# Optimization experiments

Hardware: AMD Instinct MI355X
Metric: run time of the kernel (lower is better)

Reference implementation:

```python
import jax, jax.numpy as jnp
import numpy as np
import math

B, C, H, W = 4, 256, 64, 64
E = 96  # embed_dim
SOFTMAX_SCALE = 10.0
RESIDUAL_SCALE_INIT = 0.1


def conv1x1(w, x):
    # w: [out_c, in_c], x: [b, in_c, h, w] -> [b, out_c, h, w]
    return jnp.einsum('oc,bchw->bohw', w, x)


def setup_inputs() -> dict:
    key = jax.random.key(0)
    ks = jax.random.split(key, 12)
    s = 0.02
    return {
        'x': jax.random.normal(ks[0], (B, C, H, W), jnp.float32),
        'mask': jax.random.uniform(ks[1], (B, 1, H, W), jnp.float32),
        'ln_gamma': jnp.ones((C,), jnp.float32),
        'ln_beta': jnp.zeros((C,), jnp.float32),
        'wq': jax.random.normal(ks[2], (E, C), jnp.float32) * s,
        'wk': jax.random.normal(ks[3], (E, C), jnp.float32) * s,
        'wv': jax.random.normal(ks[4], (C, C), jnp.float32) * s,
        'w_out': jax.random.normal(ks[5], (C, C), jnp.float32) * s,
        'w_qm': jax.random.normal(ks[6], (E, 1), jnp.float32) * s,
        'wd1': jax.random.normal(ks[7], (C, 2 * C), jnp.float32) * s,
        'wd2': jax.random.normal(ks[8], (C, C), jnp.float32) * s,
        'wg': jax.random.normal(ks[9], (C, C + 1), jnp.float32) * s,
        'residual_scale': jnp.asarray(RESIDUAL_SCALE_INIT, jnp.float32),
    }


def reference(x, mask, ln_gamma, ln_beta, wq, wk, wv, w_out, w_qm, wd1, wd2, wg,
              residual_scale):
    b, c, h, w = x.shape
    n = h * w

    # ChannelLayerNorm: LayerNorm over channel dim
    mu = jnp.mean(x, axis=1, keepdims=True)
    var = jnp.mean((x - mu) ** 2, axis=1, keepdims=True)
    x_norm = (x - mu) / jnp.sqrt(var + 1e-5)
    x_norm = x_norm * ln_gamma[None, :, None, None] + ln_beta[None, :, None, None]

    # Q/K/V projections (1x1 convs), flatten to [b, n, d]
    q = conv1x1(wq, x_norm) + conv1x1(w_qm, mask)
    q = q.reshape(b, E, n).transpose(0, 2, 1)        # [b, n, E]
    k = conv1x1(wk, x_norm).reshape(b, E, n).transpose(0, 2, 1)  # [b, n, E]
    v = conv1x1(wv, x).reshape(b, c, n).transpose(0, 2, 1)       # [b, n, C]

    # cosine normalization (F.normalize with eps=1e-12)
    q = q / jnp.clip(jnp.linalg.norm(q, axis=-1, keepdims=True), 1e-12)
    k = k / jnp.clip(jnp.linalg.norm(k, axis=-1, keepdims=True), 1e-12)

    scale = SOFTMAX_SCALE / math.sqrt(E)
    attn = jnp.einsum('bqe,bke->bqk', q, k) * scale  # [b, n, n]

    # keys with mask >= 0.5 are invalid -> bias -10000
    invalid_keys = (mask.reshape(b, 1, n) >= 0.5)    # [b, 1, n]
    attn = jnp.where(invalid_keys, jnp.float32(-10000.0), attn)
    attn = jax.nn.softmax(attn, axis=-1)

    attended = jnp.einsum('bqk,bkc->bqc', attn, v)   # [b, n, C]
    attended = attended.transpose(0, 2, 1).reshape(b, c, h, w)
    attended = conv1x1(w_out, attended)

    # delta correction branch
    corr_in = jnp.concatenate([attended - x, x_norm * mask], axis=1)  # [b, 2C, h, w]
    hidden = jax.nn.gelu(conv1x1(wd1, corr_in), approximate=False)
    corrective = conv1x1(wd2, hidden)

    # MaskConditionedGate (assumed): sigmoid(1x1 conv over [corrective, mask])
    gate_in = jnp.concatenate([corrective, mask], axis=1)  # [b, C+1, h, w]
    gate = jax.nn.sigmoid(conv1x1(wg, gate_in)) * mask

    delta = jnp.tanh(residual_scale) * gate * corrective
    return x + delta
```

## Files before the change

### kernel.cpp

```cpp
#include <hip/hip_runtime.h>
#include <hip/hip_bf16.h>
#include <math.h>

#define BB 4
#define CC 256
#define NN 4096
#define EE 96
#define NTOT (BB*NN)

typedef __attribute__((ext_vector_type(8))) short bf16x8;
typedef __attribute__((ext_vector_type(4))) float f32x4;

__device__ __forceinline__ short f2bf(float x) {
    __hip_bfloat16 h = __float2bfloat16(x);
    return *reinterpret_cast<short*>(&h);
}
__device__ __forceinline__ float bf2f(short s) {
    unsigned int u = ((unsigned int)(unsigned short)s) << 16;
    float f;
    __builtin_memcpy(&f, &u, 4);
    return f;
}
__device__ __forceinline__ float gelu_exact(float v) {
    return 0.5f * v * (1.0f + erff(v * 0.70710678118654752f));
}
__device__ __forceinline__ void gld16(void* lds, const void* g) {
    __builtin_amdgcn_global_load_lds(
        (const __attribute__((address_space(1))) unsigned int*)g,
        (__attribute__((address_space(3))) unsigned int*)lds, 16, 0, 0);
}

#define OFF_WQ  0
#define OFF_WK  24576
#define OFF_WV  49152
#define OFF_WO  114688
#define OFF_WD1 180224
#define OFF_WD2 311296
#define OFF_WG  376832
#define OFF_WGL 442368
#define W16_TOTAL 442624

__global__ void wconv_kernel(const float* __restrict__ wq, const float* __restrict__ wk,
                             const float* __restrict__ wv, const float* __restrict__ wo,
                             const float* __restrict__ wd1, const float* __restrict__ wd2,
                             const float* __restrict__ wg, short* __restrict__ W16) {
    int i = blockIdx.x * 256 + threadIdx.x;
    if (i >= W16_TOTAL) return;
    float v;
    if      (i < OFF_WK)  v = wq[i];
    else if (i < OFF_WV)  v = wk[i - OFF_WK];
    else if (i < OFF_WO)  v = wv[i - OFF_WV];
    else if (i < OFF_WD1) v = wo[i - OFF_WO];
    else if (i < OFF_WD2) v = wd1[i - OFF_WD1];
    else if (i < OFF_WG)  v = wd2[i - OFF_WD2];
    else if (i < OFF_WGL) { int l = i - OFF_WG; v = wg[(l >> 8) * 257 + (l & 255)]; }
    else                  v = wg[(i - OFF_WGL) * 257 + 256];
    W16[i] = f2bf(v);
}

__global__ __launch_bounds__(256) void ln_kernel(
    const float* __restrict__ x, const float* __restrict__ gamma,
    const float* __restrict__ beta,
    short* __restrict__ Xt16, short* __restrict__ Xn16) {
    __shared__ float tile[256 * 33];
    __shared__ float psum[8][32], psq[8][32];
    __shared__ float mu_s[32], rs_s[32];
    __shared__ float gs[256], bs[256];
    const int b  = blockIdx.x >> 7;
    const int p0 = (blockIdx.x & 127) * 32;
    const int tid = threadIdx.x;
    const float* xb = x + (size_t)b * CC * NN;

    gs[tid] = gamma[tid];
    bs[tid] = beta[tid];
    #pragma unroll
    for (int i = 0; i < 8; ++i) {
        int idx = tid + i * 256;
        int c = idx >> 3, p4 = (idx & 7) * 4;
        float4 v = *(const float4*)&xb[(size_t)c * NN + p0 + p4];
        tile[c * 33 + p4]     = v.x;
        tile[c * 33 + p4 + 1] = v.y;
        tile[c * 33 + p4 + 2] = v.z;
        tile[c * 33 + p4 + 3] = v.w;
    }
    __syncthreads();
    {
        int col = tid & 31, part = tid >> 5;
        float s = 0.f, sq = 0.f;
        for (int r = part * 32; r < part * 32 + 32; ++r) {
            float v = tile[r * 33 + col];
            s += v; sq += v * v;
        }
        psum[part][col] = s; psq[part][col] = sq;
    }
    __syncthreads();
    if (tid < 32) {
        float S = 0.f, SQ = 0.f;
        #pragma unroll
        for (int j = 0; j < 8; ++j) { S += psum[j][tid]; SQ += psq[j][tid]; }
        float mu = S / 256.0f;
        float var = SQ / 256.0f - mu * mu;
        mu_s[tid] = mu;
        rs_s[tid] = rsqrtf(var + 1e-5f);
    }
    __syncthreads();
    size_t rowbase = ((size_t)b * NN + p0) * CC;
    #pragma unroll
    for (int i = 0; i < 4; ++i) {
        int idx = tid + i * 256;
        int p = idx >> 5, c8 = (idx & 31) * 8;
        float mu = mu_s[p], rcp = rs_s[p];
        bf16x8 xt, xn;
        #pragma unroll
        for (int j = 0; j < 8; ++j) {
            float v = tile[(c8 + j) * 33 + p];
            float n = (v - mu) * rcp * gs[c8 + j] + bs[c8 + j];
            xt[j] = f2bf(v); xn[j] = f2bf(n);
        }
        size_t o = rowbase + (size_t)p * CC + c8;
        *(bf16x8*)&Xt16[o] = xt;
        *(bf16x8*)&Xn16[o] = xn;
    }
}

__global__ __launch_bounds__(256) void qkproj_kernel(
    const short* __restrict__ Xn16, const short* __restrict__ W16,
    const float* __restrict__ mask, const float* __restrict__ w_qm,
    short* __restrict__ Q16, short* __restrict__ K16)
{
    const int tid = threadIdx.x;
    const int w = tid >> 6, lane = tid & 63, ln = lane & 15, quad = lane >> 4;
    const int m0 = blockIdx.x * 32 + (w & 1) * 16;
    const bool isQ = (w < 2);
    const int woff = isQ ? OFF_WQ : OFF_WK;

    f32x4 acc[6];
    #pragma unroll
    for (int i = 0; i < 6; ++i) acc[i] = (f32x4){0.f, 0.f, 0.f, 0.f};

    #pragma unroll
    for (int kt = 0; kt < 8; ++kt) {
        bf16x8 af = *(const bf16x8*)&Xn16[(size_t)(m0 + ln) * 256 + kt * 32 + quad * 8];
        #pragma unroll
        for (int nt = 0; nt < 6; ++nt) {
            bf16x8 bf = *(const bf16x8*)&W16[woff + (size_t)(nt * 16 + ln) * 256 + kt * 32 + quad * 8];
            acc[nt] = __builtin_amdgcn_mfma_f32_16x16x32_bf16(af, bf, acc[nt], 0, 0, 0);
        }
    }

    short* outp = isQ ? Q16 : K16;
    #pragma unroll
    for (int r = 0; r < 4; ++r) {
        int row = m0 + quad * 4 + r;
        float mrow = isQ ? mask[row] : 0.f;
        float vals[6];
        float ss = 0.f;
        #pragma unroll
        for (int nt = 0; nt < 6; ++nt) {
            float v = acc[nt][r];
            if (isQ) v += mrow * w_qm[nt * 16 + ln];
            vals[nt] = v;
            ss += v * v;
        }
        ss += __shfl_xor(ss, 1, 64); ss += __shfl_xor(ss, 2, 64);
        ss += __shfl_xor(ss, 4, 64); ss += __shfl_xor(ss, 8, 64);
        float sc = 1.0f / fmaxf(sqrtf(ss), 1e-12f);
        #pragma unroll
        for (int nt = 0; nt < 6; ++nt)
            outp[(size_t)row * EE + nt * 16 + ln] = f2bf(vals[nt] * sc);
    }
}

__global__ __launch_bounds__(256) void vproj_kernel(
    const short* __restrict__ Xt16, const short* __restrict__ W16,
    short* __restrict__ V16t)
{
    __shared__ short Vt[256 * 40];
    const int tid = threadIdx.x;
    const int w = tid >> 6, lane = tid & 63, ln = lane & 15, quad = lane >> 4;
    const int m0 = blockIdx.x * 32;
    const int wm = w >> 1, wn = w & 1;
    const int mrow = m0 + wm * 16;

    f32x4 acc[8];
    #pragma unroll
    for (int i = 0; i < 8; ++i) acc[i] = (f32x4){0.f, 0.f, 0.f, 0.f};

    #pragma unroll
    for (int kt = 0; kt < 8; ++kt) {
        bf16x8 af = *(const bf16x8*)&Xt16[(size_t)(mrow + ln) * 256 + kt * 32 + quad * 8];
        #pragma unroll
        for (int nt = 0; nt < 8; ++nt) {
            int col = wn * 128 + nt * 16 + ln;
            bf16x8 bf = *(const bf16x8*)&W16[OFF_WV + (size_t)col * 256 + kt * 32 + quad * 8];
            acc[nt] = __builtin_amdgcn_mfma_f32_16x16x32_bf16(af, bf, acc[nt], 0, 0, 0);
        }
    }
    #pragma unroll
    for (int nt = 0; nt < 8; ++nt) {
        int ch = wn * 128 + nt * 16 + ln;
        #pragma unroll
        for (int r = 0; r < 4; ++r)
            Vt[ch * 40 + wm * 16 + quad * 4 + r] = f2bf(acc[nt][r]);
    }
    __syncthreads();
    const int b = m0 >> 12, p0l = m0 & 4095;
    #pragma unroll
    for (int i = 0; i < 4; ++i) {
        int idx = tid + i * 256;
        int ch = idx >> 2, p8 = (idx & 3) * 8;
        *(bf16x8*)&V16t[((size_t)b * CC + ch) * NN + p0l + p8] =
            *(const bf16x8*)&Vt[ch * 40 + p8];
    }
}

__global__ __launch_bounds__(256, 4) void attn_kernel(
    const short* __restrict__ Q16, const short* __restrict__ K16,
    const short* __restrict__ V16t, const float* __restrict__ mask,
    short* __restrict__ Opart, float* __restrict__ Lpart)
{
    __shared__ short Vs[8192];
    __shared__ short Ks[3072];
    __shared__ short Ps[64 * 40];
    __shared__ float flg[32];

    const int tid = threadIdx.x;
    const int w = tid >> 6, lane = tid & 63, ln = lane & 15, quad = lane >> 4;
    const int bidx = blockIdx.x;
    const int kg = bidx >> 8;
    const int qg = bidx & 255;
    const int b  = (qg & 7) >> 1;
    const int qt = ((qg >> 3) << 1) | (qg & 1);
    const int q0 = qt * 64;
    const size_t bN = (size_t)b * NN;
    const size_t bCC = (size_t)b * CC;
    const int kbase = kg * 1024;
    const float C1 = 1.02062072615966f;
    const int wbase = w * 64;

    bf16x8 qf[3];
    #pragma unroll
    for (int e = 0; e < 3; ++e)
        qf[e] = *(const bf16x8*)&Q16[(bN + q0 + w * 16 + ln) * EE + e * 32 + quad * 8];

    f32x4 acc[4][4];
    #pragma unroll
    for (int mt = 0; mt < 4; ++mt)
        #pragma unroll
        for (int nt = 0; nt < 4; ++nt) acc[mt][nt] = (f32x4){0.f, 0.f, 0.f, 0.f};
    float lsum[4] = {0.f, 0.f, 0.f, 0.f};

    gld16(&Ks[wbase * 8], &K16[(bN + kbase + (tid & 31)) * EE + (tid >> 5) * 8]);
    if (w < 2)
        gld16(&Ks[(256 + wbase) * 8],
              &K16[(bN + kbase + (tid & 31)) * EE + (8 + (tid >> 5)) * 8]);
    if (w == 3 && lane < 8)
        gld16(&flg[0], &mask[bN + kbase + lane * 4]);
    __syncthreads();

    for (int it = 0; it < 32; ++it) {
        const int k0 = kbase + it * 32;
        #pragma unroll
        for (int i = 0; i < 4; ++i)
            gld16(&Vs[(i * 256 + wbase) * 8], &V16t[(bCC + tid) * NN + k0 + i * 8]);

        f32x4 s0 = (f32x4){0.f,0.f,0.f,0.f}, s1 = s0;
        #pragma unroll
        for (int e = 0; e < 3; ++e) {
            bf16x8 kf0 = *(const bf16x8*)&Ks[((e * 4 + quad) * 32 + ln) * 8];
            bf16x8 kf1 = *(const bf16x8*)&Ks[((e * 4 + quad) * 32 + 16 + ln) * 8];
            s0 = __builtin_amdgcn_mfma_f32_16x16x32_bf16(qf[e], kf0, s0, 0, 0, 0);
            s1 = __builtin_amdgcn_mfma_f32_16x16x32_bf16(qf[e], kf1, s1, 0, 0, 0);
        }
        bool z0 = flg[ln] >= 0.5f;
        bool z1 = flg[16 + ln] >= 0.5f;
        #pragma unroll
        for (int r = 0; r < 4; ++r) {
            float p0 = z0 ? 0.f : __expf(fmaf(s0[r], C1, -C1));
            float p1 = z1 ? 0.f : __expf(fmaf(s1[r], C1, -C1));
            lsum[r] += p0 + p1;
            Ps[(w * 16 + quad * 4 + r) * 40 + ln]      = f2bf(p0);
            Ps[(w * 16 + quad * 4 + r) * 40 + 16 + ln] = f2bf(p1);
        }
        __syncthreads();

        if (it + 1 < 32) {
            const int k0n = k0 + 32;
            gld16(&Ks[wbase * 8], &K16[(bN + k0n + (tid & 31)) * EE + (tid >> 5) * 8]);
            if (w < 2)
                gld16(&Ks[(256 + wbase) * 8],
                      &K16[(bN + k0n + (tid & 31)) * EE + (8 + (tid >> 5)) * 8]);
            if (w == 3 && lane < 8)
                gld16(&flg[0], &mask[bN + k0n + lane * 4]);
        }

        #pragma unroll
        for (int mt = 0; mt < 4; ++mt) {
            bf16x8 pf = *(const bf16x8*)&Ps[(mt * 16 + ln) * 40 + quad * 8];
            #pragma unroll
            for (int nt = 0; nt < 4; ++nt) {
                bf16x8 vf = *(const bf16x8*)&Vs[(quad * 256 + wbase + nt * 16 + ln) * 8];
                acc[mt][nt] = __builtin_amdgcn_mfma_f32_16x16x32_bf16(pf, vf, acc[mt][nt], 0, 0, 0);
            }
        }
        __syncthreads();
    }

    #pragma unroll
    for (int r = 0; r < 4; ++r) {
        float l = lsum[r];
        l += __shfl_xor(l, 1, 64); l += __shfl_xor(l, 2, 64);
        l += __shfl_xor(l, 4, 64); l += __shfl_xor(l, 8, 64);
        if (ln == 0)
            Lpart[(size_t)kg * NTOT + bN + q0 + w * 16 + quad * 4 + r] = l;
    }
    #pragma unroll
    for (int mt = 0; mt < 4; ++mt)
        #pragma unroll
        for (int nt = 0; nt < 4; ++nt)
            #pragma unroll
            for (int r = 0; r < 4; ++r)
                Opart[((size_t)kg * NTOT + bN + q0 + mt * 16 + quad * 4 + r) * 256
                      + wbase + nt * 16 + ln] = f2bf(acc[mt][nt][r]);
}

__global__ __launch_bounds__(256, 2) void epi_kernel(
    const short* __restrict__ Opart, const float* __restrict__ Lpart,
    const short* __restrict__ W16, const short* __restrict__ Xt16,
    const short* __restrict__ Xn16, const float* __restrict__ mask,
    const float* __restrict__ rs, const float* __restrict__ x,
    float* __restrict__ out)
{
    __shared__ char lds[54400];
    short* Olds  = (short*)lds;
    short* Hlds  = (short*)lds;
    short* Dlds  = (short*)(lds + 16896);
    short* Clds  = (short*)(lds + 16896);
    short* tileB = (short*)(lds + 33792);
    float* lsh   = (float*)(lds + 54272);

    const int tid = threadIdx.x;
    const int w = tid >> 6, lane = tid & 63, ln = lane & 15, quad = lane >> 4;
    const int wm = w >> 1, wn = w & 1;
    const int m0 = blockIdx.x * 32;
    const int b = m0 >> 12, p0l = m0 & 4095;

    if (tid < 32) {
        int g = m0 + tid;
        lsh[tid] = 1.0f / (Lpart[g] + Lpart[NTOT + g] + Lpart[2 * NTOT + g] + Lpart[3 * NTOT + g]);
    }
    __syncthreads();

    #pragma unroll
    for (int i = 0; i < 4; ++i) {
        int idx = tid + i * 256;
        int q = idx >> 5, ch8 = (idx & 31) * 8;
        size_t base = (size_t)(m0 + q) * 256 + ch8;
        bf16x8 a0 = *(const bf16x8*)&Opart[base];
        bf16x8 a1 = *(const bf16x8*)&Opart[(size_t)NTOT * 256 + base];
        bf16x8 a2 = *(const bf16x8*)&Opart[(size_t)2 * NTOT * 256 + base];
        bf16x8 a3 = *(const bf16x8*)&Opart[(size_t)3 * NTOT * 256 + base];
        float linv = lsh[q];
        bf16x8 o;
        #pragma unroll
        for (int e = 0; e < 8; ++e)
            o[e] = f2bf((bf2f(a0[e]) + bf2f(a1[e]) + bf2f(a2[e]) + bf2f(a3[e])) * linv);
        *(bf16x8*)&Olds[q * 264 + ch8] = o;
        bf16x8 xn = *(const bf16x8*)&Xn16[base];
        float mq = mask[m0 + q];
        bf16x8 xm;
        #pragma unroll
        for (int e = 0; e < 8; ++e) xm[e] = f2bf(bf2f(xn[e]) * mq);
        *(bf16x8*)&Dlds[q * 528 + 256 + ch8] = xm;
    }
    __syncthreads();

    {
        f32x4 acc[8];
        #pragma unroll
        for (int i = 0; i < 8; ++i) acc[i] = (f32x4){0.f, 0.f, 0.f, 0.f};
        #pragma unroll
        for (int kt = 0; kt < 8; ++kt) {
            bf16x8 af = *(const bf16x8*)&Olds[(wm * 16 + ln) * 264 + kt * 32 + quad * 8];
            #pragma unroll
            for (int nt = 0; nt < 8; ++nt) {
                int col = wn * 128 + nt * 16 + ln;
                bf16x8 bf = *(const bf16x8*)&W16[OFF_WO + (size_t)col * 256 + kt * 32 + quad * 8];
                acc[nt] = __builtin_amdgcn_mfma_f32_16x16x32_bf16(af, bf, acc[nt], 0, 0, 0);
            }
        }
        #pragma unroll
        for (int nt = 0; nt < 8; ++nt) {
            int col = wn * 128 + nt * 16 + ln;
            #pragma unroll
            for (int r = 0; r < 4; ++r) {
                int row = wm * 16 + quad * 4 + r;
                float v = acc[nt][r] - bf2f(Xt16[(size_t)(m0 + row) * 256 + col]);
                Dlds[row * 528 + col] = f2bf(v);
            }
        }
    }
    __syncthreads();

    {
        f32x4 acc[8];
        #pragma unroll
        for (int i = 0; i < 8; ++i) acc[i] = (f32x4){0.f, 0.f, 0.f, 0.f};
        #pragma unroll
        for (int kt = 0; kt < 16; ++kt) {
            bf16x8 af = *(const bf16x8*)&Dlds[(wm * 16 + ln) * 528 + kt * 32 + quad * 8];
            #pragma unroll
            for (int nt = 0; nt < 8; ++nt) {
                int col = wn * 128 + nt * 16 + ln;
                bf16x8 bf = *(const bf16x8*)&W16[OFF_WD1 + (size_t)col * 512 + kt * 32 + quad * 8];
                acc[nt] = __builtin_amdgcn_mfma_f32_16x16x32_bf16(af, bf, acc[nt], 0, 0, 0);
            }
        }
        __syncthreads();
        #pragma unroll
        for (int nt = 0; nt < 8; ++nt) {
            int col = wn * 128 + nt * 16 + ln;
            #pragma unroll
            for (int r = 0; r < 4; ++r) {
                int row = wm * 16 + quad * 4 + r;
                Hlds[row * 264 + col] = f2bf(gelu_exact(acc[nt][r]));
            }
        }
    }
    __syncthreads();

    {
        f32x4 acc[8];
        #pragma unroll
        for (int i = 0; i < 8; ++i) acc[i] = (f32x4){0.f, 0.f, 0.f, 0.f};
        #pragma unroll
        for (int kt = 0; kt < 8; ++kt) {
            bf16x8 af = *(const bf16x8*)&Hlds[(wm * 16 + ln) * 264 + kt * 32 + quad * 8];
            #pragma unroll
            for (int nt = 0; nt < 8; ++nt) {
                int col = wn * 128 + nt * 16 + ln;
                bf16x8 bf = *(const bf16x8*)&W16[OFF_WD2 + (size_t)col * 256 + kt * 32 + quad * 8];
                acc[nt] = __builtin_amdgcn_mfma_f32_16x16x32_bf16(af, bf, acc[nt], 0, 0, 0);
            }
        }
        __syncthreads();
        #pragma unroll
        for (int nt = 0; nt < 8; ++nt) {
            int col = wn * 128 + nt * 16 + ln;
            #pragma unroll
            for (int r = 0; r < 4; ++r) {
                int row = wm * 16 + quad * 4 + r;
                Clds[row * 264 + col] = f2bf(acc[nt][r]);
            }
        }
    }
    __syncthreads();

    {
        f32x4 acc[8];
        #pragma unroll
        for (int i = 0; i < 8; ++i) acc[i] = (f32x4){0.f, 0.f, 0.f, 0.f};
        #pragma unroll
        for (int kt = 0; kt < 8; ++kt) {
            bf16x8 af = *(const bf16x8*)&Clds[(wm * 16 + ln) * 264 + kt * 32 + quad * 8];
            #pragma unroll
            for (int nt = 0; nt < 8; ++nt) {
                int col = wn * 128 + nt * 16 + ln;
                bf16x8 bf = *(const bf16x8*)&W16[OFF_WG + (size_t)col * 256 + kt * 32 + quad * 8];
                acc[nt] = __builtin_amdgcn_mfma_f32_16x16x32_bf16(af, bf, acc[nt], 0, 0, 0);
            }
        }
        float trs = tanhf(rs[0]);
        #pragma unroll
        for (int nt = 0; nt < 8; ++nt) {
            int col = wn * 128 + nt * 16 + ln;
            float wgl = bf2f(W16[OFF_WGL + col]);
            #pragma unroll
            for (int r = 0; r < 4; ++r) {
                int row = wm * 16 + quad * 4 + r;
                float mrow = mask[m0 + row];
                float logit = acc[nt][r] + mrow * wgl;
                float gate = mrow / (1.0f + __expf(-logit));
                float corr = bf2f(Clds[row * 264 + col]);
                tileB[col * 40 + row] = f2bf(trs * gate * corr);
            }
        }
    }
    __syncthreads();

    #pragma unroll
    for (int i = 0; i < 4; ++i) {
        int idx = tid + i * 256;
        int ch = idx >> 2, p8 = (idx & 3) * 8;
        bf16x8 d = *(const bf16x8*)&tileB[ch * 40 + p8];
        size_t o = ((size_t)b * CC + ch) * NN + p0l + p8;
        float4 x0 = *(const float4*)&x[o];
        float4 x1 = *(const float4*)&x[o + 4];
        float4 o0, o1;
        o0.x = x0.x + bf2f(d[0]); o0.y = x0.y + bf2f(d[1]);
        o0.z = x0.z + bf2f(d[2]); o0.w = x0.w + bf2f(d[3]);
        o1.x = x1.x + bf2f(d[4]); o1.y = x1.y + bf2f(d[5]);
        o1.z = x1.z + bf2f(d[6]); o1.w = x1.w + bf2f(d[7]);
        *(float4*)&out[o] = o0;
        *(float4*)&out[o + 4] = o1;
    }
}

extern "C" void kernel_launch(void* const* d_in, const int* in_sizes, int n_in,
                              void* d_out, int out_size, void* d_ws, size_t ws_size,
                              hipStream_t stream) {
    const float* x     = (const float*)d_in[0];
    const float* mask  = (const float*)d_in[1];
    const float* gamma = (const float*)d_in[2];
    const float* beta  = (const float*)d_in[3];
    const float* wq    = (const float*)d_in[4];
    const float* wk    = (const float*)d_in[5];
    const float* wv    = (const float*)d_in[6];
    const float* w_out = (const float*)d_in[7];
    const float* w_qm  = (const float*)d_in[8];
    const float* wd1   = (const float*)d_in[9];
    const float* wd2   = (const float*)d_in[10];
    const float* wg    = (const float*)d_in[11];
    const float* rs    = (const float*)d_in[12];
    float* out = (float*)d_out;

    const size_t NC = (size_t)NTOT * CC;
    const size_t NE = (size_t)NTOT * EE;
    short* Xn16  = (short*)d_ws;
    short* Xt16  = Xn16 + NC;
    short* Q16   = Xt16 + NC;
    short* K16   = Q16 + NE;
    short* V16t  = K16 + NE;
    short* W16   = V16t + NC;
    short* Opart = W16 + W16_TOTAL;
    float* Lpart = (float*)(Opart + 4 * NC);

    wconv_kernel<<<(W16_TOTAL + 255) / 256, 256, 0, stream>>>(wq, wk, wv, w_out,
                                                              wd1, wd2, wg, W16);
    ln_kernel<<<512, 256, 0, stream>>>(x, gamma, beta, Xt16, Xn16);
    qkproj_kernel<<<512, 256, 0, stream>>>(Xn16, W16, mask, w_qm, Q16, K16);
    vproj_kernel<<<512, 256, 0, stream>>>(Xt16, W16, V16t);
    attn_kernel<<<1024, 256, 0, stream>>>(Q16, K16, V16t, mask, Opart, Lpart);
    epi_kernel<<<512, 256, 0, stream>>>(Opart, Lpart, W16, Xt16, Xn16, mask,
                                        rs, x, out);
}
```

Measured before the change: 310.5 us.

## Double-buffer K tiles, load V fragments directly to registers in attention loop

The attention kernel now double-buffers the K tile in shared memory and prefetches the next tile before the QK MFMAs, not after the softmax barrier. V fragments are loaded straight from global memory into registers instead of being staged through shared memory, and the mask values are read per lane rather than through a shared flag buffer. Wave priority hints and explicit waitcnt/barrier sequencing are added around the MFMA phases. The goal is to overlap global loads with compute and cut LDS traffic, at the cost of uncoalesced, strided global V reads and more register pressure.

```diff
diff --git a/kernel.cpp b/kernel.cpp
--- a/kernel.cpp
+++ b/kernel.cpp
@@ -219,10 +219,8 @@
     const short* __restrict__ V16t, const float* __restrict__ mask,
     short* __restrict__ Opart, float* __restrict__ Lpart)
 {
-    __shared__ short Vs[8192];
-    __shared__ short Ks[3072];
+    __shared__ short Ks[2][3072];
     __shared__ short Ps[64 * 40];
-    __shared__ float flg[32];
 
     const int tid = threadIdx.x;
     const int w = tid >> 6, lane = tid & 63, ln = lane & 15, quad = lane >> 4;
@@ -250,30 +248,44 @@
         for (int nt = 0; nt < 4; ++nt) acc[mt][nt] = (f32x4){0.f, 0.f, 0.f, 0.f};
     float lsum[4] = {0.f, 0.f, 0.f, 0.f};
 
-    gld16(&Ks[wbase * 8], &K16[(bN + kbase + (tid & 31)) * EE + (tid >> 5) * 8]);
+    gld16(&Ks[0][wbase * 8], &K16[(bN + kbase + (tid & 31)) * EE + (tid >> 5) * 8]);
     if (w < 2)
-        gld16(&Ks[(256 + wbase) * 8],
+        gld16(&Ks[0][(256 + wbase) * 8],
               &K16[(bN + kbase + (tid & 31)) * EE + (8 + (tid >> 5)) * 8]);
-    if (w == 3 && lane < 8)
-        gld16(&flg[0], &mask[bN + kbase + lane * 4]);
-    __syncthreads();
-
+    __syncthreads();
+
+    int cur = 0;
     for (int it = 0; it < 32; ++it) {
         const int k0 = kbase + it * 32;
-        #pragma unroll
-        for (int i = 0; i < 4; ++i)
-            gld16(&Vs[(i * 256 + wbase) * 8], &V16t[(bCC + tid) * NN + k0 + i * 8]);
+
+        bf16x8 vf[4];
+        #pragma unroll
+        for (int nt = 0; nt < 4; ++nt)
+            vf[nt] = *(const bf16x8*)&V16t[(bCC + wbase + nt * 16 + ln) * NN + k0 + quad * 8];
+        const float mk0 = mask[bN + k0 + ln];
+        const float mk1 = mask[bN + k0 + 16 + ln];
+
+        if (it + 1 < 32) {
+            const int k0n = k0 + 32;
+            gld16(&Ks[cur ^ 1][wbase * 8],
+                  &K16[(bN + k0n + (tid & 31)) * EE + (tid >> 5) * 8]);
+            if (w < 2)
+                gld16(&Ks[cur ^ 1][(256 + wbase) * 8],
+                      &K16[(bN + k0n + (tid & 31)) * EE + (8 + (tid >> 5)) * 8]);
+        }
 
         f32x4 s0 = (f32x4){0.f,0.f,0.f,0.f}, s1 = s0;
+        __builtin_amdgcn_s_setprio(1);
         #pragma unroll
         for (int e = 0; e < 3; ++e) {
-            bf16x8 kf0 = *(const bf16x8*)&Ks[((e * 4 + quad) * 32 + ln) * 8];
-            bf16x8 kf1 = *(const bf16x8*)&Ks[((e * 4 + quad) * 32 + 16 + ln) * 8];
+            bf16x8 kf0 = *(const bf16x8*)&Ks[cur][((e * 4 + quad) * 32 + ln) * 8];
+            bf16x8 kf1 = *(const bf16x8*)&Ks[cur][((e * 4 + quad) * 32 + 16 + ln) * 8];
             s0 = __builtin_amdgcn_mfma_f32_16x16x32_bf16(qf[e], kf0, s0, 0, 0, 0);
             s1 = __builtin_amdgcn_mfma_f32_16x16x32_bf16(qf[e], kf1, s1, 0, 0, 0);
         }
-        bool z0 = flg[ln] >= 0.5f;
-        bool z1 = flg[16 + ln] >= 0.5f;
+        __builtin_amdgcn_s_setprio(0);
+        const bool z0 = mk0 >= 0.5f;
+        const bool z1 = mk1 >= 0.5f;
         #pragma unroll
         for (int r = 0; r < 4; ++r) {
             float p0 = z0 ? 0.f : __expf(fmaf(s0[r], C1, -C1));
@@ -282,28 +294,23 @@
             Ps[(w * 16 + quad * 4 + r) * 40 + ln]      = f2bf(p0);
             Ps[(w * 16 + quad * 4 + r) * 40 + 16 + ln] = f2bf(p1);
         }
-        __syncthreads();
-
-        if (it + 1 < 32) {
-            const int k0n = k0 + 32;
-            gld16(&Ks[wbase * 8], &K16[(bN + k0n + (tid & 31)) * EE + (tid >> 5) * 8]);
-            if (w < 2)
-                gld16(&Ks[(256 + wbase) * 8],
-                      &K16[(bN + k0n + (tid & 31)) * EE + (8 + (tid >> 5)) * 8]);
-            if (w == 3 && lane < 8)
-                gld16(&flg[0], &mask[bN + k0n + lane * 4]);
-        }
-
+        asm volatile("s_waitcnt lgkmcnt(0)" ::: "memory");
+        __builtin_amdgcn_s_barrier();
+        __builtin_amdgcn_sched_barrier(0);
+
+        __builtin_amdgcn_s_setprio(1);
         #pragma unroll
         for (int mt = 0; mt < 4; ++mt) {
             bf16x8 pf = *(const bf16x8*)&Ps[(mt * 16 + ln) * 40 + quad * 8];
             #pragma unroll
-            for (int nt = 0; nt < 4; ++nt) {
-                bf16x8 vf = *(const bf16x8*)&Vs[(quad * 256 + wbase + nt * 16 + ln) * 8];
-                acc[mt][nt] = __builtin_amdgcn_mfma_f32_16x16x32_bf16(pf, vf, acc[mt][nt], 0, 0, 0);
-            }
-        }
-        __syncthreads();
+            for (int nt = 0; nt < 4; ++nt)
+                acc[mt][nt] = __builtin_amdgcn_mfma_f32_16x16x32_bf16(pf, vf[nt], acc[mt][nt], 0, 0, 0);
+        }
+        __builtin_amdgcn_s_setprio(0);
+        asm volatile("s_waitcnt vmcnt(0) lgkmcnt(0)" ::: "memory");
+        __builtin_amdgcn_s_barrier();
+        __builtin_amdgcn_sched_barrier(0);
+        cur ^= 1;
     }
 
     #pragma unroll
```

Measured after the change: 300.9 us. -3.1%, faster.
